# Optimization experiments

Measured on AMD Instinct MI355X. Metric: run time of the kernel, lower is better.

Reference implementation:

```python
import jax, jax.numpy as jnp
import numpy as np

N_NODES = 100000


def setup_inputs() -> dict:
    key = jax.random.key(0)
    ks = jax.random.split(key, 8)
    N, E, Din, Dout = N_NODES, 1600000, 64, 64
    node_h = jax.random.normal(ks[0], (N, Din), jnp.float32)
    edge_h = jax.random.normal(ks[1], (E, Din), jnp.float32)
    src = jax.random.randint(ks[2], (E,), 0, N, dtype=jnp.int32)
    dst = jax.random.randint(ks[3], (E,), 0, N, dtype=jnp.int32)
    # xavier-ish scale for 64x64 weights
    s = float(np.sqrt(2.0 / (Din + Dout)))
    W_fc = jax.random.normal(ks[4], (Dout, Din), jnp.float32) * s
    W_fcr = jax.random.normal(ks[5], (Dout, Din), jnp.float32) * s
    loop_W = jax.random.normal(ks[6], (Dout, Dout), jnp.float32) * s
    return {"node_h": node_h, "edge_h": edge_h, "src": src, "dst": dst,
            "W_fc": W_fc, "W_fcr": W_fcr, "loop_W": loop_W}


def _segment_softmax(e, dst, num_segments):
    # per-destination, per-feature-channel softmax over incoming edges
    m = jax.ops.segment_max(e, dst, num_segments=num_segments)  # (N, D)
    m = jnp.where(jnp.isfinite(m), m, 0.0)  # empty segments -> -inf guard
    ex = jnp.exp(e - m[dst])                # (E, D)
    denom = jax.ops.segment_sum(ex, dst, num_segments=num_segments)
    return ex / denom[dst]


def reference(node_h, edge_h, src, dst, W_fc, W_fcr, loop_W):
    N = node_h.shape[0]
    h = node_h @ W_fc.T      # (N, Dout)  g.ndata['h'] = fc(h)
    eh = edge_h @ W_fcr.T    # (E, Dout)  g.edata['h'] = fc_r(h)
    # NOTE: original computes attn_fc(cat(src,dst,edge)) into edata['e'], but
    # message_func overwrites mailbox 'e' with edges.data['h'], so the attn_fc
    # score never reaches the output -> dead code, omitted here.
    # mailbox: z = h[src], e = r_h = eh ; alpha = softmax over mailbox dim (in-edges)
    alpha = _segment_softmax(eh, dst, N)                       # (E, Dout)
    z = h[src]                                                  # gather src feats
    agg = jax.ops.segment_sum(alpha * (z + eh), dst, num_segments=N)  # (N, Dout)
    deg = jax.ops.segment_sum(jnp.ones((dst.shape[0],), h.dtype), dst,
                              num_segments=N)
    # DGL only runs reduce on nodes with incoming messages; others keep fc(h)
    h_new = jnp.where((deg > 0)[:, None], agg + h @ loop_W, h)
    return jax.nn.relu(h_new)
```

## Files before the change

### kernel.cpp

```cpp
#include <hip/hip_runtime.h>

#define DIM 64

__global__ __launch_bounds__(256) void fc_rows(const float* __restrict__ X,
                                               const float* __restrict__ W,
                                               float* __restrict__ Y,
                                               int nrows) {
    int r = blockIdx.x * blockDim.x + threadIdx.x;
    if (r >= nrows) return;
    const float* x = X + (size_t)r * DIM;
    float4 xv[16];
#pragma unroll
    for (int i = 0; i < 16; ++i)
        xv[i] = reinterpret_cast<const float4*>(x)[i];
    float* y = Y + (size_t)r * DIM;
#pragma unroll 1
    for (int c0 = 0; c0 < DIM; c0 += 4) {
        float out[4];
#pragma unroll
        for (int j = 0; j < 4; ++j) {
            const float* w = W + (size_t)(c0 + j) * DIM;
            float p0 = 0.f, p1 = 0.f, p2 = 0.f, p3 = 0.f;
#pragma unroll
            for (int k = 0; k < 16; ++k) {
                float4 xx = xv[k];
                p0 += xx.x * w[4 * k + 0];
                p1 += xx.y * w[4 * k + 1];
                p2 += xx.z * w[4 * k + 2];
                p3 += xx.w * w[4 * k + 3];
            }
            out[j] = (p0 + p1) + (p2 + p3);
        }
        *reinterpret_cast<float4*>(y + c0) =
            make_float4(out[0], out[1], out[2], out[3]);
    }
}

__global__ __launch_bounds__(256) void hist(const int* __restrict__ dst,
                                            int* __restrict__ deg, int E) {
    int e = blockIdx.x * blockDim.x + threadIdx.x;
    if (e < E) atomicAdd(&deg[dst[e]], 1);
}

#define SCAN_T 1024
__global__ __launch_bounds__(SCAN_T) void scan_offsets(
    const int* __restrict__ deg, int* __restrict__ offsets,
    int* __restrict__ cursor, int N) {
    __shared__ int buf[2][SCAN_T];
    int t = threadIdx.x;
    int carry = 0;
    int nch = (N + SCAN_T - 1) / SCAN_T;
    for (int ch = 0; ch < nch; ++ch) {
        int i = ch * SCAN_T + t;
        int v = (i < N) ? deg[i] : 0;
        int pa = 0;
        buf[0][t] = v;
        __syncthreads();
        for (int off = 1; off < SCAN_T; off <<= 1) {
            int nv = buf[pa][t] + ((t >= off) ? buf[pa][t - off] : 0);
            __syncthreads();
            buf[pa ^ 1][t] = nv;
            __syncthreads();
            pa ^= 1;
        }
        int incl = buf[pa][t];
        int total = buf[pa][SCAN_T - 1];
        __syncthreads();
        if (i < N) {
            int ex = carry + incl - v;
            offsets[i] = ex;
            cursor[i] = ex;
        }
        carry += total;
    }
}

__global__ __launch_bounds__(256) void scatter(const int* __restrict__ src,
                                               const int* __restrict__ dst,
                                               int* __restrict__ cursor,
                                               int* __restrict__ perm,
                                               int* __restrict__ srcs, int E) {
    int e = blockIdx.x * blockDim.x + threadIdx.x;
    if (e < E) {
        int d = dst[e];
        int p = atomicAdd(&cursor[d], 1);
        perm[p] = e;
        srcs[p] = src[e];
    }
}

__global__ __launch_bounds__(256) void reduce_nodes(
    const float* __restrict__ EH, const float* __restrict__ H,
    const float* __restrict__ Wr, const float* __restrict__ LW,
    const int* __restrict__ offsets, const int* __restrict__ deg,
    const int* __restrict__ perm, const int* __restrict__ srcs,
    float* __restrict__ out, int N) {
    __shared__ float xrow[4][DIM];
    int wid = threadIdx.x >> 6;
    int lane = threadIdx.x & 63;
    int n = blockIdx.x * 4 + wid;
    if (n >= N) return;
    float* myx = xrow[wid];

    float wr[DIM];
#pragma unroll
    for (int k4 = 0; k4 < 16; ++k4) {
        float4 w = *reinterpret_cast<const float4*>(Wr + (size_t)lane * DIM + 4 * k4);
        wr[4 * k4 + 0] = w.x;
        wr[4 * k4 + 1] = w.y;
        wr[4 * k4 + 2] = w.z;
        wr[4 * k4 + 3] = w.w;
    }

    int start = offsets[n];
    int cnt = deg[n];
    float num = 0.f, den = 0.f;

    float xv_nxt = 0.f, z_nxt = 0.f;
    if (cnt > 0) {
        int e0 = perm[start];
        int s0 = srcs[start];
        xv_nxt = EH[(size_t)e0 * DIM + lane];
        z_nxt = H[(size_t)s0 * DIM + lane];
    }
#pragma unroll 1
    for (int j = 0; j < cnt; ++j) {
        float xv = xv_nxt, z = z_nxt;
        myx[lane] = xv;
        if (j + 1 < cnt) {
            int e2 = perm[start + j + 1];
            int s2 = srcs[start + j + 1];
            xv_nxt = EH[(size_t)e2 * DIM + lane];
            z_nxt = H[(size_t)s2 * DIM + lane];
        }
        asm volatile("s_waitcnt lgkmcnt(0)" ::: "memory");
        float eh = 0.f;
#pragma unroll
        for (int k4 = 0; k4 < 16; ++k4) {
            float4 x4 = *reinterpret_cast<const float4*>(myx + 4 * k4);
            eh += x4.x * wr[4 * k4 + 0];
            eh += x4.y * wr[4 * k4 + 1];
            eh += x4.z * wr[4 * k4 + 2];
            eh += x4.w * wr[4 * k4 + 3];
        }
        float ex = __expf(eh);
        num += ex * (z + eh);
        den += ex;
    }

    float hval = H[(size_t)n * DIM + lane];
    float res;
    if (cnt > 0) {
        myx[lane] = hval;
        asm volatile("s_waitcnt lgkmcnt(0)" ::: "memory");
        float loop = 0.f;
#pragma unroll
        for (int k4 = 0; k4 < 16; ++k4) {
            float4 x4 = *reinterpret_cast<const float4*>(myx + 4 * k4);
            loop += x4.x * LW[(4 * k4 + 0) * DIM + lane];
            loop += x4.y * LW[(4 * k4 + 1) * DIM + lane];
            loop += x4.z * LW[(4 * k4 + 2) * DIM + lane];
            loop += x4.w * LW[(4 * k4 + 3) * DIM + lane];
        }
        res = num / den + loop;
    } else {
        res = hval;
    }
    out[(size_t)n * DIM + lane] = fmaxf(res, 0.f);
}

extern "C" void kernel_launch(void* const* d_in, const int* in_sizes, int n_in,
                              void* d_out, int out_size, void* d_ws,
                              size_t ws_size, hipStream_t stream) {
    const float* node_h = (const float*)d_in[0];
    const float* edge_h = (const float*)d_in[1];
    const int* src = (const int*)d_in[2];
    const int* dst = (const int*)d_in[3];
    const float* W_fc = (const float*)d_in[4];
    const float* W_fcr = (const float*)d_in[5];
    const float* loop_W = (const float*)d_in[6];

    const int N = in_sizes[0] / DIM;
    const int E = in_sizes[1] / DIM;

    float* out = (float*)d_out;

    float* h = (float*)d_ws;
    int* deg = (int*)(h + (size_t)N * DIM);
    int* offsets = deg + N;
    int* cursor = offsets + N;
    int* perm = cursor + N;
    int* srcs = perm + E;

    hipMemsetAsync(deg, 0, (size_t)N * sizeof(int), stream);

    fc_rows<<<(N + 255) / 256, 256, 0, stream>>>(node_h, W_fc, h, N);
    hist<<<(E + 255) / 256, 256, 0, stream>>>(dst, deg, E);
    scan_offsets<<<1, SCAN_T, 0, stream>>>(deg, offsets, cursor, N);
    scatter<<<(E + 255) / 256, 256, 0, stream>>>(src, dst, cursor, perm, srcs, E);
    reduce_nodes<<<(N + 3) / 4, 256, 0, stream>>>(edge_h, h, W_fcr, loop_W,
                                                  offsets, deg, perm, srcs, out, N);
}
```

Before: 1.474 ms.

## Deepen edge-gather prefetch pipeline, parallelize offset scan, pack edge indices

Replaces the single-block serial prefix scan with a three-kernel multi-block scan. Packs the permuted edge id and source id into one int2 array. Restructures the per-node reduction loop to keep eight edges' feature gathers in flight using register ring buffers. This hides gather latency and removes a serial bottleneck, at the cost of more registers and extra kernel launches.

```diff
diff --git a/kernel.cpp b/kernel.cpp
--- a/kernel.cpp
+++ b/kernel.cpp
@@ -1,6 +1,7 @@
 #include <hip/hip_runtime.h>
 
 #define DIM 64
+#define UN 8
 
 __global__ __launch_bounds__(256) void fc_rows(const float* __restrict__ X,
                                                const float* __restrict__ W,
@@ -42,50 +43,68 @@
     if (e < E) atomicAdd(&deg[dst[e]], 1);
 }
 
-#define SCAN_T 1024
-__global__ __launch_bounds__(SCAN_T) void scan_offsets(
-    const int* __restrict__ deg, int* __restrict__ offsets,
-    int* __restrict__ cursor, int N) {
-    __shared__ int buf[2][SCAN_T];
+#define S1_T 1024
+__global__ __launch_bounds__(S1_T) void scan1(const int* __restrict__ deg,
+                                              int* __restrict__ incl,
+                                              int* __restrict__ bsum, int N) {
+    __shared__ int buf[2][S1_T];
     int t = threadIdx.x;
-    int carry = 0;
-    int nch = (N + SCAN_T - 1) / SCAN_T;
-    for (int ch = 0; ch < nch; ++ch) {
-        int i = ch * SCAN_T + t;
-        int v = (i < N) ? deg[i] : 0;
-        int pa = 0;
-        buf[0][t] = v;
-        __syncthreads();
-        for (int off = 1; off < SCAN_T; off <<= 1) {
-            int nv = buf[pa][t] + ((t >= off) ? buf[pa][t - off] : 0);
-            __syncthreads();
-            buf[pa ^ 1][t] = nv;
-            __syncthreads();
-            pa ^= 1;
-        }
-        int incl = buf[pa][t];
-        int total = buf[pa][SCAN_T - 1];
-        __syncthreads();
-        if (i < N) {
-            int ex = carry + incl - v;
-            offsets[i] = ex;
-            cursor[i] = ex;
-        }
-        carry += total;
+    int i = blockIdx.x * S1_T + t;
+    int v = (i < N) ? deg[i] : 0;
+    buf[0][t] = v;
+    __syncthreads();
+    int pa = 0;
+    for (int off = 1; off < S1_T; off <<= 1) {
+        int nv = buf[pa][t] + ((t >= off) ? buf[pa][t - off] : 0);
+        __syncthreads();
+        buf[pa ^ 1][t] = nv;
+        __syncthreads();
+        pa ^= 1;
+    }
+    if (i < N) incl[i] = buf[pa][t];
+    if (t == S1_T - 1) bsum[blockIdx.x] = buf[pa][t];
+}
+
+__global__ __launch_bounds__(1024) void scan2(const int* __restrict__ bsum,
+                                              int* __restrict__ boff, int G) {
+    __shared__ int buf[2][1024];
+    int t = threadIdx.x;
+    int v = (t < G) ? bsum[t] : 0;
+    buf[0][t] = v;
+    __syncthreads();
+    int pa = 0;
+    for (int off = 1; off < 1024; off <<= 1) {
+        int nv = buf[pa][t] + ((t >= off) ? buf[pa][t - off] : 0);
+        __syncthreads();
+        buf[pa ^ 1][t] = nv;
+        __syncthreads();
+        pa ^= 1;
+    }
+    if (t < G) boff[t] = buf[pa][t] - v;
+}
+
+__global__ __launch_bounds__(256) void scan3(const int* __restrict__ deg,
+                                             const int* __restrict__ incl,
+                                             const int* __restrict__ boff,
+                                             int* __restrict__ offsets,
+                                             int* __restrict__ cursor, int N) {
+    int i = blockIdx.x * blockDim.x + threadIdx.x;
+    if (i < N) {
+        int ex = incl[i] - deg[i] + boff[i >> 10];
+        offsets[i] = ex;
+        cursor[i] = ex;
     }
 }
 
 __global__ __launch_bounds__(256) void scatter(const int* __restrict__ src,
                                                const int* __restrict__ dst,
                                                int* __restrict__ cursor,
-                                               int* __restrict__ perm,
-                                               int* __restrict__ srcs, int E) {
+                                               int2* __restrict__ es, int E) {
     int e = blockIdx.x * blockDim.x + threadIdx.x;
     if (e < E) {
         int d = dst[e];
         int p = atomicAdd(&cursor[d], 1);
-        perm[p] = e;
-        srcs[p] = src[e];
+        es[p] = make_int2(e, src[e]);
     }
 }
 
@@ -93,8 +112,7 @@
     const float* __restrict__ EH, const float* __restrict__ H,
     const float* __restrict__ Wr, const float* __restrict__ LW,
     const int* __restrict__ offsets, const int* __restrict__ deg,
-    const int* __restrict__ perm, const int* __restrict__ srcs,
-    float* __restrict__ out, int N) {
+    const int2* __restrict__ es, float* __restrict__ out, int N) {
     __shared__ float xrow[4][DIM];
     int wid = threadIdx.x >> 6;
     int lane = threadIdx.x & 63;
@@ -105,7 +123,8 @@
     float wr[DIM];
 #pragma unroll
     for (int k4 = 0; k4 < 16; ++k4) {
-        float4 w = *reinterpret_cast<const float4*>(Wr + (size_t)lane * DIM + 4 * k4);
+        float4 w =
+            *reinterpret_cast<const float4*>(Wr + (size_t)lane * DIM + 4 * k4);
         wr[4 * k4 + 0] = w.x;
         wr[4 * k4 + 1] = w.y;
         wr[4 * k4 + 2] = w.z;
@@ -116,36 +135,69 @@
     int cnt = deg[n];
     float num = 0.f, den = 0.f;
 
-    float xv_nxt = 0.f, z_nxt = 0.f;
-    if (cnt > 0) {
-        int e0 = perm[start];
-        int s0 = srcs[start];
-        xv_nxt = EH[(size_t)e0 * DIM + lane];
-        z_nxt = H[(size_t)s0 * DIM + lane];
-    }
-#pragma unroll 1
-    for (int j = 0; j < cnt; ++j) {
-        float xv = xv_nxt, z = z_nxt;
-        myx[lane] = xv;
-        if (j + 1 < cnt) {
-            int e2 = perm[start + j + 1];
-            int s2 = srcs[start + j + 1];
-            xv_nxt = EH[(size_t)e2 * DIM + lane];
-            z_nxt = H[(size_t)s2 * DIM + lane];
-        }
-        asm volatile("s_waitcnt lgkmcnt(0)" ::: "memory");
-        float eh = 0.f;
-#pragma unroll
-        for (int k4 = 0; k4 < 16; ++k4) {
-            float4 x4 = *reinterpret_cast<const float4*>(myx + 4 * k4);
-            eh += x4.x * wr[4 * k4 + 0];
-            eh += x4.y * wr[4 * k4 + 1];
-            eh += x4.z * wr[4 * k4 + 2];
-            eh += x4.w * wr[4 * k4 + 3];
-        }
-        float ex = __expf(eh);
-        num += ex * (z + eh);
-        den += ex;
+    int2 eb[UN];
+    float xb[UN], zb[UN];
+
+#pragma unroll
+    for (int u = 0; u < UN; ++u) {
+        if (u < cnt) {
+            int2 q = es[start + u];
+            xb[u] = EH[(size_t)q.x * DIM + lane];
+            zb[u] = H[(size_t)q.y * DIM + lane];
+        }
+    }
+#pragma unroll
+    for (int u = 0; u < UN; ++u)
+        if (u + UN < cnt) eb[u] = es[start + u + UN];
+
+    int j = 0;
+    for (; j + UN <= cnt; j += UN) {
+#pragma unroll
+        for (int u = 0; u < UN; ++u) {
+            float xv = xb[u], z = zb[u];
+            int ridx = j + u + UN;
+            if (ridx < cnt) {
+                int2 q = eb[u];
+                xb[u] = EH[(size_t)q.x * DIM + lane];
+                zb[u] = H[(size_t)q.y * DIM + lane];
+            }
+            int iidx = j + u + 2 * UN;
+            if (iidx < cnt) eb[u] = es[start + iidx];
+            myx[lane] = xv;
+            asm volatile("s_waitcnt lgkmcnt(0)" ::: "memory");
+            float eh = 0.f;
+#pragma unroll
+            for (int k4 = 0; k4 < 16; ++k4) {
+                float4 x4 = *reinterpret_cast<const float4*>(myx + 4 * k4);
+                eh += x4.x * wr[4 * k4 + 0];
+                eh += x4.y * wr[4 * k4 + 1];
+                eh += x4.z * wr[4 * k4 + 2];
+                eh += x4.w * wr[4 * k4 + 3];
+            }
+            float ex = __expf(eh);
+            num += ex * (z + eh);
+            den += ex;
+        }
+    }
+#pragma unroll
+    for (int u = 0; u < UN; ++u) {
+        if (j + u < cnt) {
+            float xv = xb[u], z = zb[u];
+            myx[lane] = xv;
+            asm volatile("s_waitcnt lgkmcnt(0)" ::: "memory");
+            float eh = 0.f;
+#pragma unroll
+            for (int k4 = 0; k4 < 16; ++k4) {
+                float4 x4 = *reinterpret_cast<const float4*>(myx + 4 * k4);
+                eh += x4.x * wr[4 * k4 + 0];
+                eh += x4.y * wr[4 * k4 + 1];
+                eh += x4.z * wr[4 * k4 + 2];
+                eh += x4.w * wr[4 * k4 + 3];
+            }
+            float ex = __expf(eh);
+            num += ex * (z + eh);
+            den += ex;
+        }
     }
 
     float hval = H[(size_t)n * DIM + lane];
@@ -189,15 +241,21 @@
     int* deg = (int*)(h + (size_t)N * DIM);
     int* offsets = deg + N;
     int* cursor = offsets + N;
-    int* perm = cursor + N;
-    int* srcs = perm + E;
+    int* incl = cursor + N;
+    int* bsum = incl + N;
+    int* boff = bsum + 1024;
+    int2* es = (int2*)(boff + 1024);
 
     hipMemsetAsync(deg, 0, (size_t)N * sizeof(int), stream);
 
     fc_rows<<<(N + 255) / 256, 256, 0, stream>>>(node_h, W_fc, h, N);
     hist<<<(E + 255) / 256, 256, 0, stream>>>(dst, deg, E);
-    scan_offsets<<<1, SCAN_T, 0, stream>>>(deg, offsets, cursor, N);
-    scatter<<<(E + 255) / 256, 256, 0, stream>>>(src, dst, cursor, perm, srcs, E);
+    int G = (N + S1_T - 1) / S1_T;
+    scan1<<<G, S1_T, 0, stream>>>(deg, incl, bsum, N);
+    scan2<<<1, 1024, 0, stream>>>(bsum, boff, G);
+    scan3<<<(N + 255) / 256, 256, 0, stream>>>(deg, incl, boff, offsets, cursor,
+                                               N);
+    scatter<<<(E + 255) / 256, 256, 0, stream>>>(src, dst, cursor, es, E);
     reduce_nodes<<<(N + 3) / 4, 256, 0, stream>>>(edge_h, h, W_fcr, loop_W,
-                                                  offsets, deg, perm, srcs, out, N);
-}
+                                                  offsets, deg, es, out, N);
+}
```

After: 4.088 ms. 177% more time.
